# Kernel tuning notes

Hardware: AMD Instinct MI355X
Metric: run time of the kernel (lower is better)

## Reference

```python
import jax, jax.numpy as jnp
import numpy as np

B, TX, TY, C, H = 2, 1024, 4096, 768, 12
D = C // H  # head_dim = 64


def setup_inputs() -> dict:
    key = jax.random.key(0)
    ks = jax.random.split(key, 7)
    x = jax.random.normal(ks[0], (B, TX, C), dtype=jnp.float32)
    y = jax.random.normal(ks[1], (B, TY, C), dtype=jnp.float32)
    # sorted float timestamps in [0, TY]
    x_t = jnp.sort(jax.random.uniform(ks[2], (B, TX), dtype=jnp.float32) * TY, axis=-1)
    y_t = jnp.sort(jax.random.uniform(ks[3], (B, TY), dtype=jnp.float32) * TY, axis=-1)
    y_t = y_t.at[:, 0].set(0.0)  # guarantee every query sees >=1 valid key
    Wq = jax.random.normal(ks[4], (C, C), dtype=jnp.float32) * 0.02
    Wkv = jax.random.normal(ks[5], (C, 2 * C), dtype=jnp.float32) * 0.02
    Wproj = jax.random.normal(ks[6], (C, C), dtype=jnp.float32) * 0.02
    # RotaryEmbedding(dim=D, learned_freq=True): init values are the standard inv freqs
    inv_freq = 1.0 / (10000.0 ** (jnp.arange(0, D, 2, dtype=jnp.float32) / D))
    return {"x": x, "x_t": x_t, "y": y, "y_t": y_t, "dist": 512, "min_dist": 0,
            "Wq": Wq, "Wkv": Wkv, "Wproj": Wproj, "inv_freq": inv_freq}


def _rotate_half(t):
    # interleaved pair rotation: (x1, x2) -> (-x2, x1)
    p = t.reshape(t.shape[:-1] + (-1, 2))
    x1, x2 = p[..., 0], p[..., 1]
    return jnp.stack((-x2, x1), axis=-1).reshape(t.shape)


def _apply_rope(t, pos, inv_freq):
    # t: (B,H,T,D), pos: (B,T), inv_freq: (D/2,)
    f = pos[:, None, :, None] * inv_freq          # (B,1,T,D/2)
    f = jnp.repeat(f, 2, axis=-1)                 # (B,1,T,D) interleaved
    return t * jnp.cos(f) + _rotate_half(t) * jnp.sin(f)


def reference(x, x_t, y, y_t, dist, min_dist, Wq, Wkv, Wproj, inv_freq):
    q = (x @ Wq).reshape(B, TX, H, D).transpose(0, 2, 1, 3)   # (B,H,TX,D)
    kv = y @ Wkv
    k = kv[..., :C].reshape(B, TY, H, D).transpose(0, 2, 1, 3)
    v = kv[..., C:].reshape(B, TY, H, D).transpose(0, 2, 1, 3)
    q = _apply_rope(q, x_t, inv_freq)
    k = _apply_rope(k, y_t, inv_freq)
    # time-window mask: valid iff (x_t - min_dist) >= y_t and (x_t - min_dist) <= y_t + dist
    xt = (x_t - min_dist)[:, :, None]             # (B,TX,1)
    yt = y_t[:, None, :]                          # (B,1,TY)
    mask = (xt >= yt) & (xt <= yt + dist)         # (B,TX,TY)
    scores = jnp.einsum('bhqd,bhkd->bhqk', q, k) / jnp.sqrt(jnp.float32(D))
    scores = jnp.where(mask[:, None, :, :], scores, -jnp.inf)
    attn = jax.nn.softmax(scores, axis=-1)
    out = jnp.einsum('bhqk,bhkd->bhqd', attn, v)
    out = out.transpose(0, 2, 1, 3).reshape(B, TX, C)
    return out @ Wproj
```

## Files before the change

kernel.cpp:

```cpp
#include <hip/hip_runtime.h>
#include <hip/hip_bf16.h>
#include <math.h>

#define B_ 2
#define TX_ 1024
#define TY_ 4096
#define C_ 768
#define H_ 12
#define D_ 64
#define NSPLIT 4
#define R_ (B_ * H_ * TX_)

typedef __bf16 bf16x8 __attribute__((ext_vector_type(8)));
typedef float floatx4 __attribute__((ext_vector_type(4)));

__device__ __forceinline__ void async_copy16(const void* g, void* l) {
    __builtin_amdgcn_global_load_lds(
        (const __attribute__((address_space(1))) unsigned int*)g,
        (__attribute__((address_space(3))) unsigned int*)l,
        16, 0, 0);
}

__device__ __forceinline__ bf16x8 cvt8(const float* s) {
    bf16x8 r;
#pragma unroll
    for (int i = 0; i < 8; i++) r[i] = (__bf16)s[i];
    return r;
}

__global__ __launch_bounds__(256)
void prep(const float* __restrict__ x,  __bf16* __restrict__ xb,
          const float* __restrict__ y,  __bf16* __restrict__ yb,
          const float* __restrict__ Wq, __bf16* __restrict__ Wqt,
          const float* __restrict__ Wkv,__bf16* __restrict__ Wkvt,
          const float* __restrict__ Wpr,__bf16* __restrict__ Wprt)
{
    __shared__ float tile[32][33];
    const int bid = blockIdx.x;
    if (bid >= 2304) {
        const int cb = bid - 2304;
        const float* src; __bf16* dst; size_t base;
        if (cb < 768) { src = x; dst = xb; base = (size_t)cb * 2048; }
        else          { src = y; dst = yb; base = (size_t)(cb - 768) * 2048; }
        const size_t i = base + threadIdx.x * 8;
        float4 v0 = *(const float4*)(src + i);
        float4 v1 = *(const float4*)(src + i + 4);
        bf16x8 p;
        p[0] = (__bf16)v0.x; p[1] = (__bf16)v0.y; p[2] = (__bf16)v0.z; p[3] = (__bf16)v0.w;
        p[4] = (__bf16)v1.x; p[5] = (__bf16)v1.y; p[6] = (__bf16)v1.z; p[7] = (__bf16)v1.w;
        *(bf16x8*)(dst + i) = p;
        return;
    }
    const int bxr = bid % 96;
    const int byr = bid / 96;
    const float* W; __bf16* Wt; int N, nb; float scale = 1.0f;
    if (bxr < 24)      { W = Wq;  Wt = Wqt;  N = C_;     nb = bxr;      scale = 0.125f; }
    else if (bxr < 72) { W = Wkv; Wt = Wkvt; N = 2 * C_; nb = bxr - 24; }
    else               { W = Wpr; Wt = Wprt; N = C_;     nb = bxr - 72; }
    const int bx = nb * 32;
    const int by = byr * 32;
    const int tx = threadIdx.x & 31, ty = threadIdx.x >> 5;
#pragma unroll
    for (int i = 0; i < 4; i++)
        tile[ty + i * 8][tx] = W[(size_t)(by + ty + i * 8) * N + bx + tx];
    __syncthreads();
#pragma unroll
    for (int i = 0; i < 4; i++)
        Wt[(size_t)(bx + ty + i * 8) * C_ + by + tx] =
            (__bf16)(tile[tx][ty + i * 8] * scale);
}

__global__ __launch_bounds__(256)
void gemm_qkv(const __bf16* __restrict__ xb, const __bf16* __restrict__ Wqt,
              const __bf16* __restrict__ yb, const __bf16* __restrict__ Wkvt,
              __bf16* __restrict__ Qbh, __bf16* __restrict__ Kbh,
              __bf16* __restrict__ Vtb,
              const float* __restrict__ x_t, const float* __restrict__ y_t,
              const float* __restrict__ inv_freq)
{
    const int bid = blockIdx.x;
    const bool isQ = (bid < 192);
    const __bf16* A; const __bf16* Bt; const float* t_arr;
    int row0, n0, T, TSH;
    if (isQ) {
        A = xb; Bt = Wqt; t_arr = x_t;
        row0 = (bid / 6) * 64; n0 = (bid % 6) * 128; T = TX_; TSH = 10;
    } else {
        const int r = bid - 192;
        A = yb; Bt = Wkvt; t_arr = y_t;
        row0 = (r / 12) * 64; n0 = (r % 12) * 128; T = TY_; TSH = 12;
    }
    const bool isV = (!isQ) && (n0 >= C_);

    __shared__ __align__(16) float smem_f[6144];
    __bf16* smem_b = (__bf16*)smem_f;

    const int tid  = threadIdx.x;
    const int wave = tid >> 6;
    const int lane = tid & 63;
    const int m16  = lane & 15;
    const int quad = lane >> 4;
    const int wm   = wave >> 1;
    const int wn   = wave & 1;

    floatx4 acc[2][4];
#pragma unroll
    for (int i = 0; i < 2; i++)
#pragma unroll
        for (int j = 0; j < 4; j++) acc[i][j] = (floatx4){0.f, 0.f, 0.f, 0.f};

    const int eA = wave * 512 + lane * 8;
    const int srA = eA >> 5, scA = eA & 31;
    int srB[2], scB[2];
#pragma unroll
    for (int j = 0; j < 2; j++) {
        const int e = j * 2048 + wave * 512 + lane * 8;
        srB[j] = e >> 5; scB[j] = e & 31;
    }

    for (int k0 = 0; k0 < C_; k0 += 64) {
        __syncthreads();
#pragma unroll
        for (int c = 0; c < 2; c++) {
            const int kk = k0 + c * 32;
            async_copy16(A + (size_t)(row0 + srA) * C_ + (kk + scA),
                         (char*)smem_f + c * 12288 + wave * 1024);
#pragma unroll
            for (int j = 0; j < 2; j++)
                async_copy16(Bt + (size_t)(n0 + srB[j]) * C_ + (kk + scB[j]),
                             (char*)smem_f + c * 12288 + 4096 + j * 4096 + wave * 1024);
        }
        __syncthreads();

#pragma unroll
        for (int c = 0; c < 2; c++) {
            const __bf16* As = smem_b + c * 6144;
            const __bf16* Bs = As + 2048;
            bf16x8 af[2], bfr[4];
#pragma unroll
            for (int i = 0; i < 2; i++)
                af[i] = *(const bf16x8*)(As + (size_t)(wm * 32 + i * 16 + m16) * 32 + quad * 8);
#pragma unroll
            for (int j = 0; j < 4; j++)
                bfr[j] = *(const bf16x8*)(Bs + (size_t)(wn * 64 + j * 16 + m16) * 32 + quad * 8);
#pragma unroll
            for (int i = 0; i < 2; i++)
#pragma unroll
                for (int j = 0; j < 4; j++)
                    acc[i][j] = __builtin_amdgcn_mfma_f32_16x16x32_bf16(af[i], bfr[j], acc[i][j], 0, 0, 0);
        }
    }

    const int STR = 132;
    float* fs = smem_f;

#pragma unroll
    for (int i = 0; i < 2; i++) {
        __syncthreads();
#pragma unroll
        for (int j = 0; j < 4; j++) {
            const int col_l = wn * 64 + j * 16 + m16;
#pragma unroll
            for (int r = 0; r < 4; r++) {
                const int row_l = quad * 4 + r;
                float v = acc[i][j][r];
                if (!isV) {
                    const float vp = __shfl_xor(v, 1);
                    const int row = row0 + wm * 32 + i * 16 + row_l;
                    const int cc = (n0 + col_l) & (D_ - 1);
                    const float fr = t_arr[row] * inv_freq[cc >> 1];
                    const float sn = __sinf(fr), cs = __cosf(fr);
                    v = (m16 & 1) ? (v * cs + vp * sn) : (v * cs - vp * sn);
                }
                fs[(wm * 16 + row_l) * STR + col_l] = v;
            }
        }
        __syncthreads();

        if (!isV) {
            __bf16* outb = isQ ? Qbh : Kbh;
            const int r32 = tid >> 3;
            const int lane8 = tid & 7;
            const int grow = row0 + (r32 >> 4) * 32 + i * 16 + (r32 & 15);
            const int bb = grow >> TSH;
            const int rk = grow & (T - 1);
            const int h  = (n0 >> 6) + (lane8 >> 2);
            const int d0 = (lane8 & 3) * 16;
            __bf16* gp = outb + ((size_t)(bb * H_ + h) * T + rk) * 64 + d0;
            const float* sp = &fs[r32 * STR + lane8 * 16];
            *(bf16x8*)gp       = cvt8(sp);
            *(bf16x8*)(gp + 8) = cvt8(sp + 8);
        } else {
            const int dcol = tid >> 1;
            const int g16  = tid & 1;
            const int h  = ((n0 - C_) >> 6) + (dcol >> 6);
            const int dd = dcol & 63;
            const int kbase = row0 + g16 * 32 + i * 16;
            const int bb  = kbase >> 12;
            const int kin = kbase & (TY_ - 1);
            float tmp[16];
#pragma unroll
            for (int jj = 0; jj < 16; jj++)
                tmp[jj] = fs[(g16 * 16 + jj) * STR + dcol];
            __bf16* gp = Vtb + ((size_t)(bb * H_ + h) * 64 + dd) * TY_ + kin;
            *(bf16x8*)gp       = cvt8(tmp);
            *(bf16x8*)(gp + 8) = cvt8(tmp + 8);
        }
    }
}

__global__ __launch_bounds__(256)
void attn_mfma(const __bf16* __restrict__ Qb,
               const __bf16* __restrict__ Kb,
               const __bf16* __restrict__ Vt,
               const float* __restrict__ x_t,
               const float* __restrict__ y_t,
               const int* __restrict__ dist_p,
               const int* __restrict__ min_dist_p,
               float* __restrict__ pacc,
               float* __restrict__ pml)
{
    __shared__ __align__(16) __bf16 Kc[32 * 64];
    __shared__ __align__(16) __bf16 Vc[64 * 32];
    __shared__ __align__(16) __bf16 Pt[4][16 * 32];

    const int tid  = threadIdx.x;
    const int wave = tid >> 6;
    const int m16  = tid & 15;
    const int quad = (tid & 63) >> 4;
    const int qt = blockIdx.x, bh = blockIdx.y, split = blockIdx.z;
    const int b = bh / H_;
    const int qblk  = qt * 64;
    const int qbase = qblk + wave * 16;

    const float dist = (float)dist_p[0];
    const float md   = (float)min_dist_p[0];
    const float* yt = y_t + (size_t)b * TY_;
    const float* xt = x_t + (size_t)b * TX_;

    const float xtmin = xt[qblk] - md;
    const float xtmax = xt[qblk + 63] - md;
    int lo = 0, hi = TY_;
    while (lo < hi) { int mid = (lo + hi) >> 1; if (yt[mid] + dist < xtmin) lo = mid + 1; else hi = mid; }
    const int klo = lo;
    lo = 0; hi = TY_;
    while (lo < hi) { int mid = (lo + hi) >> 1; if (yt[mid] <= xtmax) lo = mid + 1; else hi = mid; }
    const int khi = lo - 1;
    const int len = khi - klo + 1;

    int k0 = klo, k1 = klo;
    if (len > 0) {
        const int cnt = (len + NSPLIT - 1) / NSPLIT;
        k0 = klo + split * cnt;
        k1 = min(k0 + cnt, klo + len);
    }

    float xtq[4];
#pragma unroll
    for (int r = 0; r < 4; r++)
        xtq[r] = xt[qbase + quad * 4 + r] - md;

    const __bf16* qp = Qb + ((size_t)bh * TX_ + qbase + m16) * 64;
    const bf16x8 aq0 = *(const bf16x8*)(qp + quad * 8);
    const bf16x8 aq1 = *(const bf16x8*)(qp + 32 + quad * 8);

    float l[4];
    floatx4 o[4];
#pragma unroll
    for (int r = 0; r < 4; r++) l[r] = 0.f;
#pragma unroll
    for (int t = 0; t < 4; t++) o[t] = (floatx4){0.f, 0.f, 0.f, 0.f};

    for (int kc = k0; kc < k1; kc += 32) {
        const float yt0 = yt[min(kc + m16, TY_ - 1)];
        const float yt1 = yt[min(kc + 16 + m16, TY_ - 1)];

        __syncthreads();
        {
            const int krow = tid >> 3;
            const int kg = min(kc + krow, TY_ - 1);
            async_copy16(Kb + ((size_t)bh * TY_ + kg) * 64 + (tid & 7) * 8,
                         (char*)Kc + tid * 16);
            const int d = tid >> 2;
            const int kv = min(kc + (tid & 3) * 8, TY_ - 8);
            async_copy16(Vt + ((size_t)bh * 64 + d) * TY_ + kv,
                         (char*)Vc + tid * 16);
        }
        __syncthreads();

        const bf16x8 bk0h0 = *(const bf16x8*)(Kc + m16 * 64 + quad * 8);
        const bf16x8 bk1h0 = *(const bf16x8*)(Kc + m16 * 64 + 32 + quad * 8);
        const bf16x8 bk0h1 = *(const bf16x8*)(Kc + (16 + m16) * 64 + quad * 8);
        const bf16x8 bk1h1 = *(const bf16x8*)(Kc + (16 + m16) * 64 + 32 + quad * 8);
        floatx4 s0 = (floatx4){0.f, 0.f, 0.f, 0.f};
        floatx4 s1 = (floatx4){0.f, 0.f, 0.f, 0.f};
        s0 = __builtin_amdgcn_mfma_f32_16x16x32_bf16(aq0, bk0h0, s0, 0, 0, 0);
        s0 = __builtin_amdgcn_mfma_f32_16x16x32_bf16(aq1, bk1h0, s0, 0, 0, 0);
        s1 = __builtin_amdgcn_mfma_f32_16x16x32_bf16(aq0, bk0h1, s1, 0, 0, 0);
        s1 = __builtin_amdgcn_mfma_f32_16x16x32_bf16(aq1, bk1h1, s1, 0, 0, 0);

        const int kg0 = kc + m16;
        const int kg1 = kc + 16 + m16;
        __bf16* pt = Pt[wave];
#pragma unroll
        for (int r = 0; r < 4; r++) {
            const bool v0 = (kg0 < k1) && (xtq[r] >= yt0) && (xtq[r] <= yt0 + dist);
            const bool v1 = (kg1 < k1) && (xtq[r] >= yt1) && (xtq[r] <= yt1 + dist);
            const float p0 = v0 ? (float)(__bf16)__expf(s0[r]) : 0.f;
            const float p1 = v1 ? (float)(__bf16)__expf(s1[r]) : 0.f;
            l[r] += p0 + p1;
            pt[(quad * 4 + r) * 32 + m16]      = (__bf16)p0;
            pt[(quad * 4 + r) * 32 + 16 + m16] = (__bf16)p1;
        }
        const bf16x8 ap = *(const bf16x8*)(pt + m16 * 32 + quad * 8);
#pragma unroll
        for (int t = 0; t < 4; t++) {
            const bf16x8 bv = *(const bf16x8*)(Vc + (t * 16 + m16) * 32 + quad * 8);
            o[t] = __builtin_amdgcn_mfma_f32_16x16x32_bf16(ap, bv, o[t], 0, 0, 0);
        }
    }

#pragma unroll
    for (int r = 0; r < 4; r++) {
#pragma unroll
        for (int w = 1; w < 16; w <<= 1)
            l[r] += __shfl_xor(l[r], w);
    }

#pragma unroll
    for (int t = 0; t < 4; t++)
#pragma unroll
        for (int r = 0; r < 4; r++) {
            const size_t gr = (size_t)bh * TX_ + qbase + quad * 4 + r;
            pacc[((size_t)split * R_ + gr) * 64 + t * 16 + m16] = o[t][r];
        }
    if (m16 == 0) {
#pragma unroll
        for (int r = 0; r < 4; r++) {
            const size_t gr = (size_t)bh * TX_ + qbase + quad * 4 + r;
            pml[(size_t)split * R_ + gr] = l[r];
        }
    }
}

__global__ __launch_bounds__(256)
void combine_kernel(const float* __restrict__ pacc,
                    const float* __restrict__ pml,
                    __bf16* __restrict__ O)
{
    const int d   = threadIdx.x;
    const int sub = threadIdx.y;
    const size_t r = (size_t)blockIdx.x * 4 + sub;
    const int bh  = (int)(r / TX_);
    const int txg = (int)(r % TX_);
    const int b = bh / H_, h = bh % H_;

    float L = 0.f, val = 0.f;
#pragma unroll
    for (int s = 0; s < NSPLIT; s++) {
        L   += pml[(size_t)s * R_ + r];
        val += pacc[((size_t)s * R_ + r) * 64 + d];
    }
    const float o = (L > 0.f) ? val / L : 0.f;
    O[(size_t)(b * TX_ + txg) * C_ + h * D_ + d] = (__bf16)o;
}

__global__ __launch_bounds__(256)
void gemm_proj(const __bf16* __restrict__ A,
               const __bf16* __restrict__ Bt,
               float* __restrict__ out0)
{
    __shared__ __align__(16) float smem_f[8192];
    __bf16* smem_b = (__bf16*)smem_f;

    const int tid  = threadIdx.x;
    const int wave = tid >> 6;
    const int lane = tid & 63;
    const int m16  = lane & 15;
    const int quad = lane >> 4;
    const int wm   = wave >> 1;
    const int wn   = wave & 1;
    const int row0 = blockIdx.y * 128;
    const int n0   = blockIdx.x * 128;

    floatx4 acc[4][4];
#pragma unroll
    for (int i = 0; i < 4; i++)
#pragma unroll
        for (int j = 0; j < 4; j++) acc[i][j] = (floatx4){0.f, 0.f, 0.f, 0.f};

    int srow[4], scol[4];
#pragma unroll
    for (int j = 0; j < 4; j++) {
        int e = j * 2048 + wave * 512 + lane * 8;
        int e2 = e & 4095;
        srow[j] = e2 >> 5;
        scol[j] = e2 & 31;
    }

    for (int k0 = 0; k0 < C_; k0 += 64) {
        __syncthreads();
#pragma unroll
        for (int c = 0; c < 2; c++) {
            const int kk = k0 + c * 32;
#pragma unroll
            for (int j = 0; j < 4; j++) {
                const __bf16* src = (j < 2)
                    ? A  + (size_t)(row0 + srow[j]) * C_ + (kk + scol[j])
                    : Bt + (size_t)(n0   + srow[j]) * C_ + (kk + scol[j]);
                async_copy16(src, (char*)smem_f + c * 16384 + j * 4096 + wave * 1024);
            }
        }
        __syncthreads();

#pragma unroll
        for (int c = 0; c < 2; c++) {
            const __bf16* As = smem_b + c * 8192;
            const __bf16* Bs = As + 4096;
            bf16x8 af[4], bfr[4];
#pragma unroll
            for (int i = 0; i < 4; i++)
                af[i] = *(const bf16x8*)(As + (size_t)(wm * 64 + i * 16 + m16) * 32 + quad * 8);
#pragma unroll
            for (int j = 0; j < 4; j++)
                bfr[j] = *(const bf16x8*)(Bs + (size_t)(wn * 64 + j * 16 + m16) * 32 + quad * 8);
#pragma unroll
            for (int i = 0; i < 4; i++)
#pragma unroll
                for (int j = 0; j < 4; j++)
                    acc[i][j] = __builtin_amdgcn_mfma_f32_16x16x32_bf16(af[i], bfr[j], acc[i][j], 0, 0, 0);
        }
    }

    const int STR = 132;
    float* fs = smem_f;
#pragma unroll
    for (int i = 0; i < 4; i++) {
        __syncthreads();
#pragma unroll
        for (int j = 0; j < 4; j++) {
            const int col_l = wn * 64 + j * 16 + m16;
#pragma unroll
            for (int r = 0; r < 4; r++)
                fs[(wm * 16 + quad * 4 + r) * STR + col_l] = acc[i][j][r];
        }
        __syncthreads();
        const int r32 = tid >> 3;
        const int lc  = (tid & 7) * 4;
        const int row = row0 + (r32 >> 4) * 64 + i * 16 + (r32 & 15);
        float* gp = out0 + (size_t)row * C_ + n0;
#pragma unroll
        for (int c2 = 0; c2 < 4; c2++) {
            float4 v4 = *(const float4*)&fs[r32 * STR + c2 * 32 + lc];
            *(float4*)(gp + c2 * 32 + lc) = v4;
        }
    }
}

extern "C" void kernel_launch(void* const* d_in, const int* in_sizes, int n_in,
                              void* d_out, int out_size, void* d_ws, size_t ws_size,
                              hipStream_t stream)
{
    const float* x        = (const float*)d_in[0];
    const float* x_t      = (const float*)d_in[1];
    const float* y        = (const float*)d_in[2];
    const float* y_t      = (const float*)d_in[3];
    const int*   dist     = (const int*)d_in[4];
    const int*   min_dist = (const int*)d_in[5];
    const float* Wq       = (const float*)d_in[6];
    const float* Wkv      = (const float*)d_in[7];
    const float* Wproj    = (const float*)d_in[8];
    const float* inv_freq = (const float*)d_in[9];
    float* out = (float*)d_out;

    const size_t QN = (size_t)B_ * TX_ * C_;
    const size_t KN = (size_t)B_ * TY_ * C_;

    float* ws = (float*)d_ws;
    float* pacc = ws; ws += (size_t)NSPLIT * R_ * 64;
    float* pml  = ws; ws += (size_t)NSPLIT * R_;
    __bf16* bws = (__bf16*)ws;
    __bf16* xb    = bws; bws += QN;
    __bf16* yb    = bws; bws += KN;
    __bf16* Wqt   = bws; bws += (size_t)C_ * C_;
    __bf16* Wkvt  = bws; bws += (size_t)C_ * 2 * C_;
    __bf16* Wprt  = bws; bws += (size_t)C_ * C_;
    __bf16* Ob    = bws; bws += QN;
    __bf16* Qbh   = bws; bws += QN;
    __bf16* Kbh   = bws; bws += KN;
    __bf16* Vtb   = bws; bws += KN + 128;

    prep<<<dim3(2304 + 3840), dim3(256), 0, stream>>>(
        x, xb, y, yb, Wq, Wqt, Wkv, Wkvt, Wproj, Wprt);

    gemm_qkv<<<dim3(1728), dim3(256), 0, stream>>>(
        xb, Wqt, yb, Wkvt, Qbh, Kbh, Vtb, x_t, y_t, inv_freq);

    attn_mfma<<<dim3(TX_ / 64, B_ * H_, NSPLIT), dim3(256), 0, stream>>>(
        Qbh, Kbh, Vtb, x_t, y_t, dist, min_dist, pacc, pml);

    combine_kernel<<<dim3((unsigned)(R_ / 4)), dim3(64, 4), 0, stream>>>(
        pacc, pml, Ob);

    gemm_proj<<<dim3(C_ / 128, (B_ * TX_) / 128), dim3(256), 0, stream>>>(
        Ob, Wprt, out);
}
```

Measured before the change: 200.4 us.

## Triple-buffer async LDS loads in QKV and projection GEMMs

Result: faster. 194.7 us (-2.8%).

```diff
diff --git a/kernel.cpp b/kernel.cpp
--- a/kernel.cpp
+++ b/kernel.cpp
@@ -92,7 +92,7 @@
     }
     const bool isV = (!isQ) && (n0 >= C_);
 
-    __shared__ __align__(16) float smem_f[6144];
+    __shared__ __align__(16) float smem_f[9216];
     __bf16* smem_b = (__bf16*)smem_f;
 
     const int tid  = threadIdx.x;
@@ -118,37 +118,47 @@
         srB[j] = e >> 5; scB[j] = e & 31;
     }
 
-    for (int k0 = 0; k0 < C_; k0 += 64) {
-        __syncthreads();
-#pragma unroll
-        for (int c = 0; c < 2; c++) {
-            const int kk = k0 + c * 32;
-            async_copy16(A + (size_t)(row0 + srA) * C_ + (kk + scA),
-                         (char*)smem_f + c * 12288 + wave * 1024);
-#pragma unroll
-            for (int j = 0; j < 2; j++)
-                async_copy16(Bt + (size_t)(n0 + srB[j]) * C_ + (kk + scB[j]),
-                             (char*)smem_f + c * 12288 + 4096 + j * 4096 + wave * 1024);
-        }
-        __syncthreads();
-
-#pragma unroll
-        for (int c = 0; c < 2; c++) {
-            const __bf16* As = smem_b + c * 6144;
-            const __bf16* Bs = As + 2048;
-            bf16x8 af[2], bfr[4];
-#pragma unroll
-            for (int i = 0; i < 2; i++)
-                af[i] = *(const bf16x8*)(As + (size_t)(wm * 32 + i * 16 + m16) * 32 + quad * 8);
+    auto stage = [&](int chunk, int buf) {
+        const int kk = chunk * 32;
+        async_copy16(A + (size_t)(row0 + srA) * C_ + (kk + scA),
+                     (char*)smem_f + buf * 12288 + wave * 1024);
+#pragma unroll
+        for (int j = 0; j < 2; j++)
+            async_copy16(Bt + (size_t)(n0 + srB[j]) * C_ + (kk + scB[j]),
+                         (char*)smem_f + buf * 12288 + 4096 + j * 4096 + wave * 1024);
+    };
+
+    stage(0, 0);
+    stage(1, 1);
+
+    int cur = 0;
+    for (int t = 0; t < 24; ++t) {
+        if (t < 23) asm volatile("s_waitcnt vmcnt(3)" ::: "memory");
+        else        asm volatile("s_waitcnt vmcnt(0)" ::: "memory");
+        __builtin_amdgcn_s_barrier();
+        asm volatile("" ::: "memory");
+
+        if (t + 2 < 24) {
+            int nb = cur + 2; if (nb >= 3) nb -= 3;
+            stage(t + 2, nb);
+        }
+
+        const __bf16* As = smem_b + cur * 6144;
+        const __bf16* Bs = As + 2048;
+        bf16x8 af[2], bfr[4];
+#pragma unroll
+        for (int i = 0; i < 2; i++)
+            af[i] = *(const bf16x8*)(As + (size_t)(wm * 32 + i * 16 + m16) * 32 + quad * 8);
+#pragma unroll
+        for (int j = 0; j < 4; j++)
+            bfr[j] = *(const bf16x8*)(Bs + (size_t)(wn * 64 + j * 16 + m16) * 32 + quad * 8);
+#pragma unroll
+        for (int i = 0; i < 2; i++)
 #pragma unroll
             for (int j = 0; j < 4; j++)
-                bfr[j] = *(const bf16x8*)(Bs + (size_t)(wn * 64 + j * 16 + m16) * 32 + quad * 8);
-#pragma unroll
-            for (int i = 0; i < 2; i++)
-#pragma unroll
-                for (int j = 0; j < 4; j++)
-                    acc[i][j] = __builtin_amdgcn_mfma_f32_16x16x32_bf16(af[i], bfr[j], acc[i][j], 0, 0, 0);
-        }
+                acc[i][j] = __builtin_amdgcn_mfma_f32_16x16x32_bf16(af[i], bfr[j], acc[i][j], 0, 0, 0);
+
+        cur = (cur == 2) ? 0 : cur + 1;
     }
 
     const int STR = 132;
@@ -370,7 +380,7 @@
                const __bf16* __restrict__ Bt,
                float* __restrict__ out0)
 {
-    __shared__ __align__(16) float smem_f[8192];
+    __shared__ __align__(16) float smem_f[12288];
     __bf16* smem_b = (__bf16*)smem_f;
 
     const int tid  = threadIdx.x;
@@ -398,38 +408,48 @@
         scol[j] = e2 & 31;
     }
 
-    for (int k0 = 0; k0 < C_; k0 += 64) {
-        __syncthreads();
-#pragma unroll
-        for (int c = 0; c < 2; c++) {
-            const int kk = k0 + c * 32;
-#pragma unroll
-            for (int j = 0; j < 4; j++) {
-                const __bf16* src = (j < 2)
-                    ? A  + (size_t)(row0 + srow[j]) * C_ + (kk + scol[j])
-                    : Bt + (size_t)(n0   + srow[j]) * C_ + (kk + scol[j]);
-                async_copy16(src, (char*)smem_f + c * 16384 + j * 4096 + wave * 1024);
-            }
-        }
-        __syncthreads();
-
-#pragma unroll
-        for (int c = 0; c < 2; c++) {
-            const __bf16* As = smem_b + c * 8192;
-            const __bf16* Bs = As + 4096;
-            bf16x8 af[4], bfr[4];
-#pragma unroll
-            for (int i = 0; i < 4; i++)
-                af[i] = *(const bf16x8*)(As + (size_t)(wm * 64 + i * 16 + m16) * 32 + quad * 8);
+    auto stage = [&](int chunk, int buf) {
+        const int kk = chunk * 32;
+#pragma unroll
+        for (int j = 0; j < 4; j++) {
+            const __bf16* src = (j < 2)
+                ? A  + (size_t)(row0 + srow[j]) * C_ + (kk + scol[j])
+                : Bt + (size_t)(n0   + srow[j]) * C_ + (kk + scol[j]);
+            async_copy16(src, (char*)smem_f + buf * 16384 + j * 4096 + wave * 1024);
+        }
+    };
+
+    stage(0, 0);
+    stage(1, 1);
+
+    int cur = 0;
+    for (int t = 0; t < 24; ++t) {
+        if (t < 23) asm volatile("s_waitcnt vmcnt(4)" ::: "memory");
+        else        asm volatile("s_waitcnt vmcnt(0)" ::: "memory");
+        __builtin_amdgcn_s_barrier();
+        asm volatile("" ::: "memory");
+
+        if (t + 2 < 24) {
+            int nb = cur + 2; if (nb >= 3) nb -= 3;
+            stage(t + 2, nb);
+        }
+
+        const __bf16* As = smem_b + cur * 8192;
+        const __bf16* Bs = As + 4096;
+        bf16x8 af[4], bfr[4];
+#pragma unroll
+        for (int i = 0; i < 4; i++)
+            af[i] = *(const bf16x8*)(As + (size_t)(wm * 64 + i * 16 + m16) * 32 + quad * 8);
+#pragma unroll
+        for (int j = 0; j < 4; j++)
+            bfr[j] = *(const bf16x8*)(Bs + (size_t)(wn * 64 + j * 16 + m16) * 32 + quad * 8);
+#pragma unroll
+        for (int i = 0; i < 4; i++)
 #pragma unroll
             for (int j = 0; j < 4; j++)
-                bfr[j] = *(const bf16x8*)(Bs + (size_t)(wn * 64 + j * 16 + m16) * 32 + quad * 8);
-#pragma unroll
-            for (int i = 0; i < 4; i++)
-#pragma unroll
-                for (int j = 0; j < 4; j++)
-                    acc[i][j] = __builtin_amdgcn_mfma_f32_16x16x32_bf16(af[i], bfr[j], acc[i][j], 0, 0, 0);
-        }
+                acc[i][j] = __builtin_amdgcn_mfma_f32_16x16x32_bf16(af[i], bfr[j], acc[i][j], 0, 0, 0);
+
+        cur = (cur == 2) ? 0 : cur + 1;
     }
 
     const int STR = 132;
```
